# Kernel optimization log

Hardware: AMD Instinct MI355X
Metric: run time of the kernel (lower is better)

The kernel has to match this reference:

```python
import jax, jax.numpy as jnp
import numpy as np

D_MODEL = 1024
N_HEAD = 16
D_K = D_MODEL // N_HEAD


def setup_inputs() -> dict:
    key = jax.random.key(0)
    ks = jax.random.split(key, 11)
    B, S = 2, 2048
    std = 1.0 / np.sqrt(D_MODEL)
    inp = {
        "Q": jax.random.normal(ks[0], (B, S, D_MODEL), jnp.float32),
        "K": jax.random.normal(ks[1], (B, S, D_MODEL), jnp.float32),
        "V": jax.random.normal(ks[2], (B, S, D_MODEL), jnp.float32),
        "Wq": jax.random.normal(ks[3], (D_MODEL, D_MODEL), jnp.float32) * std,
        "bq": jnp.zeros((D_MODEL,), jnp.float32),
        "Wk": jax.random.normal(ks[4], (D_MODEL, D_MODEL), jnp.float32) * std,
        "bk": jnp.zeros((D_MODEL,), jnp.float32),
        "Wv": jax.random.normal(ks[5], (D_MODEL, D_MODEL), jnp.float32) * std,
        "bv": jnp.zeros((D_MODEL,), jnp.float32),
        "Wo": jax.random.normal(ks[6], (D_MODEL, D_MODEL), jnp.float32) * std,
        "bo": jnp.zeros((D_MODEL,), jnp.float32),
    }
    return inp


def _split_heads(x):
    # [B, S, D] -> [B, H, S, d_k]
    B, S, _ = x.shape
    return x.reshape(B, S, N_HEAD, D_K).transpose(0, 2, 1, 3)


def reference(Q, K, V, Wq, bq, Wk, bk, Wv, bv, Wo, bo):
    q = _split_heads(Q @ Wq.T + bq)   # [B,H,S,dk]
    k = _split_heads(K @ Wk.T + bk)
    v = _split_heads(V @ Wv.T + bv)
    scale = 1.0 / jnp.sqrt(jnp.float32(D_K))
    scores = jnp.einsum("bhqd,bhkd->bhqk", q, k) * scale
    attn = jax.nn.softmax(scores, axis=-1)
    ctx = jnp.einsum("bhqk,bhkd->bhqd", attn, v)  # [B,H,S,dk]
    B, H, S, dk = ctx.shape
    ctx = ctx.transpose(0, 2, 1, 3).reshape(B, S, H * dk)
    return ctx @ Wo.T + bo
```

## Files before the change

### kernel.cpp

```cpp
#include <hip/hip_runtime.h>
#include <hip/hip_bf16.h>
#include <cstdint>
#include <cstddef>
#include <cmath>

typedef __attribute__((ext_vector_type(8))) short short8;
typedef __attribute__((ext_vector_type(4))) short short4_t;
typedef __attribute__((ext_vector_type(4))) float f32x4;
typedef __attribute__((ext_vector_type(16))) float f32x16;

constexpr int B_ = 2, S_ = 2048, H_ = 16, DK_ = 64, DM_ = 1024;

__device__ inline unsigned short f2bf(float x) {
  union { float f; unsigned u; } c; c.f = x;
  unsigned r = c.u + 0x7FFF + ((c.u >> 16) & 1);
  return (unsigned short)(r >> 16);
}

__device__ inline float ex2(float x) {
#if __has_builtin(__builtin_amdgcn_exp2f)
  return __builtin_amdgcn_exp2f(x);
#else
  return exp2f(x);
#endif
}

__device__ inline unsigned pkbf(float lo, float hi) {
  unsigned u;
  asm("v_cvt_pk_bf16_f32 %0, %1, %2" : "=v"(u) : "v"(lo), "v"(hi));
  return u;
}

__device__ inline void plswap(unsigned& a, unsigned& b) {
#if __has_builtin(__builtin_amdgcn_permlane32_swap)
  auto r = __builtin_amdgcn_permlane32_swap(a, b, false, false);
  a = (unsigned)r[0];
  b = (unsigned)r[1];
#else
  unsigned sa = __shfl_xor(a, 32), sb = __shfl_xor(b, 32);
  unsigned lid = __builtin_amdgcn_mbcnt_hi(~0u, __builtin_amdgcn_mbcnt_lo(~0u, 0));
  bool hi = lid >= 32;
  unsigned na = hi ? sb : a;
  unsigned nb = hi ? b : sa;
  a = na; b = nb;
#endif
}

__device__ inline float red_half_max(float x) {
  unsigned a = __float_as_uint(x), b = a;
  plswap(a, b);
  return fmaxf(__uint_as_float(a), __uint_as_float(b));
}
__device__ inline float red_half_sum(float x) {
  unsigned a = __float_as_uint(x), b = a;
  plswap(a, b);
  return __uint_as_float(a) + __uint_as_float(b);
}

__device__ inline f32x4 mfma16(short8 a, short8 b, f32x4 c) {
  return __builtin_amdgcn_mfma_f32_16x16x32_bf16(a, b, c, 0, 0, 0);
}
__device__ inline f32x16 mfma32(short8 a, short8 b, f32x16 c) {
  return __builtin_amdgcn_mfma_f32_32x32x16_bf16(a, b, c, 0, 0, 0);
}

__device__ inline void glds16(const unsigned short* g, unsigned short* l) {
  __builtin_amdgcn_global_load_lds(
      (const __attribute__((address_space(1))) unsigned int*)g,
      (__attribute__((address_space(3))) unsigned int*)l, 16, 0, 0);
}

__global__ __launch_bounds__(256) void cvt_all(
    const float* __restrict__ Q, const float* __restrict__ K,
    const float* __restrict__ V, const float* __restrict__ Wq,
    const float* __restrict__ Wk, const float* __restrict__ Wv,
    const float* __restrict__ Wo, unsigned short* __restrict__ Qb,
    unsigned short* __restrict__ Kb, unsigned short* __restrict__ Vb,
    unsigned short* __restrict__ Wqb, unsigned short* __restrict__ Wkb,
    unsigned short* __restrict__ Wvb, unsigned short* __restrict__ Wob) {
  int bid = blockIdx.x;
  const float* in; unsigned short* out; int off;
  if (bid < 4096)       { in = Q;  out = Qb;  off = bid; }
  else if (bid < 8192)  { in = K;  out = Kb;  off = bid - 4096; }
  else if (bid < 12288) { in = V;  out = Vb;  off = bid - 8192; }
  else if (bid < 13312) { in = Wq; out = Wqb; off = bid - 12288; }
  else if (bid < 14336) { in = Wk; out = Wkb; off = bid - 13312; }
  else if (bid < 15360) { in = Wv; out = Wvb; off = bid - 14336; }
  else                  { in = Wo; out = Wob; off = bid - 15360; }
  int i = off * 256 + threadIdx.x;
  float4 f = ((const float4*)in)[i];
  uint2 o;
  o.x = pkbf(f.x, f.y);
  o.y = pkbf(f.z, f.w);
  ((uint2*)out)[i] = o;
}

__device__ inline void store_out(float* p, float v) { *p = v; }
__device__ inline void store_out(unsigned short* p, float v) { *p = f2bf(v); }

template <typename OUT_T>
__device__ inline void gemm128_body(const unsigned short* __restrict__ A,
                                    const unsigned short* __restrict__ Bw,
                                    const float* __restrict__ bias,
                                    OUT_T* __restrict__ C, float cscale,
                                    int bm, int bn) {
  constexpr int Kd = 1024, Nd = 1024;
  __shared__ unsigned short As[128][64];
  __shared__ unsigned short Bs[128][64];

  const int tid = threadIdx.x;
  const int lane = tid & 63, wave = tid >> 6;
  const int li = lane & 15, lg = lane >> 4;
  const int wm = wave >> 1, wn = wave & 1;

  const f32x4 zero4 = {0.f, 0.f, 0.f, 0.f};
  f32x4 acc[4][4];
#pragma unroll
  for (int i = 0; i < 4; i++)
#pragma unroll
    for (int j = 0; j < 4; j++) acc[i][j] = zero4;

  const int srow = tid >> 3;
  const int scol = (tid & 7) * 8;
  const unsigned short* Ag = A + (size_t)(bm * 128 + srow) * Kd + scol;
  const unsigned short* Bg = Bw + (size_t)(bn * 128 + srow) * Kd + scol;

  for (int kt = 0; kt < Kd; kt += 64) {
#pragma unroll
    for (int i = 0; i < 4; i++) {
      glds16(Ag + (size_t)(i * 32) * Kd + kt, &As[i * 32 + srow][scol]);
      glds16(Bg + (size_t)(i * 32) * Kd + kt, &Bs[i * 32 + srow][scol]);
    }
    __syncthreads();

    short8 af[4][2], bf[4][2];
#pragma unroll
    for (int kb = 0; kb < 2; kb++)
#pragma unroll
      for (int i = 0; i < 4; i++) {
        af[i][kb] = *(const short8*)&As[wm * 64 + i * 16 + li][kb * 32 + lg * 8];
        bf[i][kb] = *(const short8*)&Bs[wn * 64 + i * 16 + li][kb * 32 + lg * 8];
      }
#pragma unroll
    for (int kb = 0; kb < 2; kb++)
#pragma unroll
      for (int i = 0; i < 4; i++)
#pragma unroll
        for (int j = 0; j < 4; j++)
          acc[i][j] = mfma16(af[i][kb], bf[j][kb], acc[i][j]);
    __syncthreads();
  }

#pragma unroll
  for (int j = 0; j < 4; j++) {
    int col = bn * 128 + wn * 64 + j * 16 + li;
    float bv = bias[col];
#pragma unroll
    for (int i = 0; i < 4; i++) {
      int row0 = bm * 128 + wm * 64 + i * 16 + lg * 4;
#pragma unroll
      for (int r = 0; r < 4; r++)
        store_out(&C[(size_t)(row0 + r) * Nd + col], (acc[i][j][r] + bv) * cscale);
    }
  }
}

__global__ __launch_bounds__(256) void gemm_qkv(
    const unsigned short* __restrict__ Aq, const unsigned short* __restrict__ Ak,
    const unsigned short* __restrict__ Av, const unsigned short* __restrict__ Bq,
    const unsigned short* __restrict__ Bk, const unsigned short* __restrict__ Bv,
    const float* __restrict__ bq, const float* __restrict__ bk,
    const float* __restrict__ bv, unsigned short* __restrict__ Cq,
    unsigned short* __restrict__ Ck, unsigned short* __restrict__ Cv,
    float qscale) {
  const int z = blockIdx.z;
  const unsigned short* A = z == 0 ? Aq : z == 1 ? Ak : Av;
  const unsigned short* Bw = z == 0 ? Bq : z == 1 ? Bk : Bv;
  const float* bi = z == 0 ? bq : z == 1 ? bk : bv;
  unsigned short* C = z == 0 ? Cq : z == 1 ? Ck : Cv;
  gemm128_body(A, Bw, bi, C, z == 0 ? qscale : 1.0f, blockIdx.x, blockIdx.y);
}

__device__ inline void gemm_body(const unsigned short* __restrict__ A,
                                 const unsigned short* __restrict__ Bw,
                                 const float* __restrict__ bias,
                                 float* __restrict__ C, int bm, int bn) {
  constexpr int Kd = 1024, Nd = 1024, NSTEP = Kd / 64;
  __shared__ unsigned short As[2][128][64];
  __shared__ unsigned short Bs[2][64][64];

  const int tid = threadIdx.x;
  const int lane = tid & 63, wave = tid >> 6;
  const int li = lane & 15, lg = lane >> 4;
  const int wm = wave >> 1, wn = wave & 1;

  const f32x4 zero4 = {0.f, 0.f, 0.f, 0.f};
  f32x4 acc[4][2];
#pragma unroll
  for (int i = 0; i < 4; i++)
#pragma unroll
    for (int j = 0; j < 2; j++) acc[i][j] = zero4;

  const int stg_row = tid >> 3;
  const int stg_col = (tid & 7) * 8;
  const unsigned short* Ag = A + (size_t)(bm * 128 + stg_row) * Kd + stg_col;
  const unsigned short* Bg = Bw + (size_t)(bn * 64 + stg_row) * Kd + stg_col;

#pragma unroll
  for (int i = 0; i < 4; i++)
    glds16(Ag + (size_t)(i * 32) * Kd, &As[0][i * 32 + stg_row][stg_col]);
#pragma unroll
  for (int i = 0; i < 2; i++)
    glds16(Bg + (size_t)(i * 32) * Kd, &Bs[0][i * 32 + stg_row][stg_col]);

  for (int kt = 0; kt < NSTEP; kt++) {
    const int buf = kt & 1;
    asm volatile("s_waitcnt vmcnt(0)" ::: "memory");
    __builtin_amdgcn_sched_barrier(0);
    __builtin_amdgcn_s_barrier();
    __builtin_amdgcn_sched_barrier(0);

    if (kt + 1 < NSTEP) {
      const int kof = (kt + 1) * 64;
#pragma unroll
      for (int i = 0; i < 4; i++)
        glds16(Ag + (size_t)(i * 32) * Kd + kof,
               &As[buf ^ 1][i * 32 + stg_row][stg_col]);
#pragma unroll
      for (int i = 0; i < 2; i++)
        glds16(Bg + (size_t)(i * 32) * Kd + kof,
               &Bs[buf ^ 1][i * 32 + stg_row][stg_col]);
    }
    __builtin_amdgcn_sched_barrier(0);

    short8 af[4][2], bf[2][2];
#pragma unroll
    for (int kb = 0; kb < 2; kb++) {
#pragma unroll
      for (int i = 0; i < 4; i++)
        af[i][kb] =
            *(const short8*)&As[buf][wm * 64 + i * 16 + li][kb * 32 + lg * 8];
#pragma unroll
      for (int j = 0; j < 2; j++)
        bf[j][kb] =
            *(const short8*)&Bs[buf][wn * 32 + j * 16 + li][kb * 32 + lg * 8];
    }
#pragma unroll
    for (int kb = 0; kb < 2; kb++)
#pragma unroll
      for (int i = 0; i < 4; i++)
#pragma unroll
        for (int j = 0; j < 2; j++)
          acc[i][j] = mfma16(af[i][kb], bf[j][kb], acc[i][j]);
  }

#pragma unroll
  for (int j = 0; j < 2; j++) {
    int col = bn * 64 + wn * 32 + j * 16 + li;
    float bv = bias[col];
#pragma unroll
    for (int i = 0; i < 4; i++) {
      int row0 = bm * 128 + wm * 64 + i * 16 + lg * 4;
#pragma unroll
      for (int r = 0; r < 4; r++)
        store_out(&C[(size_t)(row0 + r) * Nd + col], acc[i][j][r] + bv);
    }
  }
}

__global__ __launch_bounds__(256, 3) void gemm_out(
    const unsigned short* __restrict__ A, const unsigned short* __restrict__ Bw,
    const float* __restrict__ bias, float* __restrict__ C) {
  gemm_body(A, Bw, bias, C, blockIdx.x, blockIdx.y);
}

struct V4 { short8 v[4]; };

__device__ __forceinline__ void attn_tile_step(
    int kt, int buf, int NT,
    const unsigned short* kg, const unsigned short* vg,
    unsigned short* KsAll, unsigned short* VtAll,
    int srow, int sc, int scs, int key2, int dq,
    const short8* qf, int l31, int h,
    V4& vc, V4& vn, f32x16* po, float& m_i, float& l_i) {
  unsigned short* KsB = KsAll + buf * (128 * 64);
  unsigned short* VtB = VtAll + buf * (64 * 128);
  unsigned short* KsO = KsAll + (buf ^ 1) * (128 * 64);

  asm volatile("s_waitcnt vmcnt(0)" ::: "memory");
  __builtin_amdgcn_sched_barrier(0);

#pragma unroll
  for (int j = 0; j < 16; j++) {
    const int half = j >> 3, jj = j & 7;
    unsigned w = (unsigned)(unsigned short)vc.v[half][jj] |
                 ((unsigned)(unsigned short)vc.v[2 + half][jj] << 16);
    const int slot = (key2 >> 3) ^ j;
    *(unsigned*)&VtB[(dq * 16 + j) * 128 + slot * 8 + (key2 & 7)] = w;
  }

  if (kt + 1 < NT) {
    const unsigned short* vp =
        vg + (size_t)((kt + 1) * 128 + key2) * DM_ + dq * 16;
    vn.v[0] = *(const short8*)(vp);
    vn.v[1] = *(const short8*)(vp + 8);
    vn.v[2] = *(const short8*)(vp + DM_);
    vn.v[3] = *(const short8*)(vp + DM_ + 8);
  }

  asm volatile("s_waitcnt lgkmcnt(0)" ::: "memory");
  __builtin_amdgcn_sched_barrier(0);
  __builtin_amdgcn_s_barrier();
  __builtin_amdgcn_sched_barrier(0);

  if (kt + 1 < NT) {
    const unsigned short* kgt = kg + (size_t)((kt + 1) * 128) * DM_;
#pragma unroll
    for (int i = 0; i < 4; i++)
      glds16(kgt + (size_t)(i * 32 + srow) * DM_ + scs,
             &KsO[(i * 32 + srow) * 64 + sc * 8]);
  }
  __builtin_amdgcn_sched_barrier(0);

  f32x16 sacc[4];
#pragma unroll
  for (int kb = 0; kb < 4; kb++)
#pragma unroll
    for (int r = 0; r < 16; r++) sacc[kb][r] = 0.f;

  __builtin_amdgcn_s_setprio(1);
#pragma unroll
  for (int tq = 0; tq < 4; tq++) {
    const int sl = ((((tq << 1) | h) ^ (l31 & 7))) * 8;
#pragma unroll
    for (int kb = 0; kb < 4; kb++) {
      short8 kf = *(const short8*)&KsB[(kb * 32 + l31) * 64 + sl];
      sacc[kb] = mfma32(kf, qf[tq], sacc[kb]);
    }
  }
  __builtin_amdgcn_s_setprio(0);

  float mx = -1e30f;
#pragma unroll
  for (int kb = 0; kb < 4; kb++)
#pragma unroll
    for (int r = 0; r < 16; r += 4)
      mx = fmaxf(mx, fmaxf(fmaxf(sacc[kb][r], sacc[kb][r + 1]),
                           fmaxf(sacc[kb][r + 2], sacc[kb][r + 3])));
  mx = red_half_max(mx);

  if (!__all(mx - m_i <= 8.0f)) {
    float mn = fmaxf(m_i, mx);
    float al = ex2(m_i - mn);
    m_i = mn;
    l_i *= al;
#pragma unroll
    for (int db = 0; db < 2; db++)
#pragma unroll
      for (int r = 0; r < 16; r++) po[db][r] *= al;
  }

  float s0 = 0.f, s1 = 0.f, s2 = 0.f, s3 = 0.f;
#pragma unroll
  for (int kb = 0; kb < 4; kb++) {
#pragma unroll
    for (int r = 0; r < 16; r += 4) {
      float p0 = ex2(sacc[kb][r] - m_i);
      float p1 = ex2(sacc[kb][r + 1] - m_i);
      float p2 = ex2(sacc[kb][r + 2] - m_i);
      float p3 = ex2(sacc[kb][r + 3] - m_i);
      sacc[kb][r] = p0; sacc[kb][r + 1] = p1;
      sacc[kb][r + 2] = p2; sacc[kb][r + 3] = p3;
      s0 += p0; s1 += p1; s2 += p2; s3 += p3;
    }
    unsigned u[4][2];
#pragma unroll
    for (int qd = 0; qd < 4; qd++) {
      u[qd][0] = pkbf(sacc[kb][4 * qd], sacc[kb][4 * qd + 1]);
      u[qd][1] = pkbf(sacc[kb][4 * qd + 2], sacc[kb][4 * qd + 3]);
    }
    __builtin_amdgcn_s_setprio(1);
#pragma unroll
    for (int tt = 0; tt < 2; tt++) {
      const int tp = 2 * kb + tt;
      unsigned x0 = u[2 * tt][0], x1 = u[2 * tt][1];
      unsigned y0 = u[2 * tt + 1][0], y1 = u[2 * tt + 1][1];
      plswap(x0, y0);
      plswap(x1, y1);
      union { unsigned w[4]; short8 v8; } fr;
      fr.w[0] = x0;
      fr.w[1] = x1;
      fr.w[2] = y0;
      fr.w[3] = y1;
      const int slbase = (tp << 1) | h;
#pragma unroll
      for (int db = 0; db < 2; db++) {
        const int row = db * 32 + l31;
        short8 vf = *(const short8*)
            &VtB[row * 128 + (slbase ^ (l31 & 15)) * 8];
        po[db] = mfma32(vf, fr.v8, po[db]);
      }
    }
    __builtin_amdgcn_s_setprio(0);
  }
  float sum = (s0 + s1) + (s2 + s3);
  l_i += red_half_sum(sum);
}

__global__ __launch_bounds__(256, 2) void attn_fwd(
    const unsigned short* __restrict__ q, const unsigned short* __restrict__ k,
    const unsigned short* __restrict__ v, unsigned short* __restrict__ ctx) {
  __shared__ unsigned short Ks[2][128][64];
  __shared__ unsigned short Vt[2][64][128];

  const int tid = threadIdx.x;
  const int lane = tid & 63, wave = tid >> 6;
  const int l31 = lane & 31, h = lane >> 5;
  const int n = blockIdx.x;
  const int xcd = n & 7, m = n >> 3;
  const int bh = xcd * 4 + (m & 3);
  const int qt = m >> 2;
  const int b = bh >> 4, hd = bh & 15;

  const int qrow = qt * 128 + wave * 32 + l31;
  const unsigned short* qg = q + (size_t)(b * S_ + qrow) * DM_ + hd * DK_;
  short8 qf[4];
#pragma unroll
  for (int t = 0; t < 4; t++) qf[t] = *(const short8*)(qg + t * 16 + h * 8);

  f32x16 po[2];
#pragma unroll
  for (int db = 0; db < 2; db++)
#pragma unroll
    for (int r = 0; r < 16; r++) po[db][r] = 0.f;
  float m_i = -1e30f, l_i = 0.f;

  const int srow = tid >> 3, sc = tid & 7;
  const int scs = (sc ^ (srow & 7)) * 8;
  const unsigned short* kg = k + (size_t)(b * S_) * DM_ + hd * DK_;

  const int key2 = (tid & 63) * 2, dq = tid >> 6;
  const unsigned short* vg = v + (size_t)(b * S_) * DM_ + hd * DK_;

  const int NT = S_ / 128;

#pragma unroll
  for (int i = 0; i < 4; i++)
    glds16(kg + (size_t)(i * 32 + srow) * DM_ + scs,
           &Ks[0][i * 32 + srow][sc * 8]);
  V4 va, vb;
  {
    const unsigned short* vp = vg + (size_t)key2 * DM_ + dq * 16;
    va.v[0] = *(const short8*)(vp);
    va.v[1] = *(const short8*)(vp + 8);
    va.v[2] = *(const short8*)(vp + DM_);
    va.v[3] = *(const short8*)(vp + DM_ + 8);
  }

  unsigned short* KsAll = &Ks[0][0][0];
  unsigned short* VtAll = &Vt[0][0][0];
  for (int it = 0; it < NT; it += 2) {
    attn_tile_step(it, 0, NT, kg, vg, KsAll, VtAll, srow, sc, scs, key2, dq,
                   qf, l31, h, va, vb, po, m_i, l_i);
    attn_tile_step(it + 1, 1, NT, kg, vg, KsAll, VtAll, srow, sc, scs, key2,
                   dq, qf, l31, h, vb, va, po, m_i, l_i);
  }

  float rl = 1.0f / l_i;
  unsigned short* cg = ctx + (size_t)(b * S_ + qrow) * DM_ + hd * DK_;
#pragma unroll
  for (int db = 0; db < 2; db++)
#pragma unroll
    for (int rq = 0; rq < 4; rq++) {
      uint2 w2;
      w2.x = pkbf(po[db][4 * rq] * rl, po[db][4 * rq + 1] * rl);
      w2.y = pkbf(po[db][4 * rq + 2] * rl, po[db][4 * rq + 3] * rl);
      *(uint2*)(cg + db * 32 + 8 * rq + 4 * h) = w2;
    }
}

extern "C" void kernel_launch(void* const* d_in, const int* in_sizes, int n_in,
                              void* d_out, int out_size, void* d_ws, size_t ws_size,
                              hipStream_t stream) {
  const float* Q  = (const float*)d_in[0];
  const float* Kx = (const float*)d_in[1];
  const float* V  = (const float*)d_in[2];
  const float* Wq = (const float*)d_in[3];
  const float* bq = (const float*)d_in[4];
  const float* Wk = (const float*)d_in[5];
  const float* bk = (const float*)d_in[6];
  const float* Wv = (const float*)d_in[7];
  const float* bv = (const float*)d_in[8];
  const float* Wo = (const float*)d_in[9];
  const float* bo = (const float*)d_in[10];
  float* out = (float*)d_out;

  char* ws = (char*)d_ws;
  const size_t MB = 1ull << 20;
  unsigned short* Qb  = (unsigned short*)(ws + 0 * MB);
  unsigned short* Kb  = (unsigned short*)(ws + 8 * MB);
  unsigned short* Vb  = (unsigned short*)(ws + 16 * MB);
  unsigned short* Wqb = (unsigned short*)(ws + 24 * MB);
  unsigned short* Wkb = (unsigned short*)(ws + 26 * MB);
  unsigned short* Wvb = (unsigned short*)(ws + 28 * MB);
  unsigned short* Wob = (unsigned short*)(ws + 30 * MB);
  unsigned short* qp  = (unsigned short*)(ws + 32 * MB);
  unsigned short* kp  = (unsigned short*)(ws + 40 * MB);
  unsigned short* vp  = (unsigned short*)(ws + 48 * MB);
  unsigned short* cx  = (unsigned short*)(ws + 56 * MB);

  cvt_all<<<16384, 256, 0, stream>>>(Q, Kx, V, Wq, Wk, Wv, Wo,
                                     Qb, Kb, Vb, Wqb, Wkb, Wvb, Wob);

  gemm_qkv<<<dim3(32, 8, 3), 256, 0, stream>>>(
      Qb, Kb, Vb, Wqb, Wkb, Wvb, bq, bk, bv, qp, kp, vp, 0.18033688f);

  attn_fwd<<<512, 256, 0, stream>>>(qp, kp, vp, cx);

  gemm_out<<<dim3(32, 16), 256, 0, stream>>>(cx, Wob, bo, out);
}
```

Before: 135.8 us.

## Split attention key tiles across two wave groups per block with LDS merge

The attention kernel now launches 512 threads per block. Two groups of four waves each process half of every 128-key tile for the same 128 query rows, which halves per-wave MFMA and softmax work per tile. Each group keeps its own running max and sum. The partial outputs are merged through LDS at the end using a log-sum-exp rescale. This adds a final sync and merge step plus extra registers per block, and it aims to raise the number of waves per CU to hide latency.

```diff
diff --git a/kernel.cpp b/kernel.cpp
--- a/kernel.cpp
+++ b/kernel.cpp
@@ -274,15 +274,15 @@
   gemm_body(A, Bw, bias, C, blockIdx.x, blockIdx.y);
 }
 
-struct V4 { short8 v[4]; };
+struct V2 { short8 v[2]; };
 
 __device__ __forceinline__ void attn_tile_step(
     int kt, int buf, int NT,
     const unsigned short* kg, const unsigned short* vg,
     unsigned short* KsAll, unsigned short* VtAll,
     int srow, int sc, int scs, int key2, int dq,
-    const short8* qf, int l31, int h,
-    V4& vc, V4& vn, f32x16* po, float& m_i, float& l_i) {
+    const short8* qf, int l31, int h, int grp,
+    V2& vc, V2& vn, f32x16* po, float& m_i, float& l_i) {
   unsigned short* KsB = KsAll + buf * (128 * 64);
   unsigned short* VtB = VtAll + buf * (64 * 128);
   unsigned short* KsO = KsAll + (buf ^ 1) * (128 * 64);
@@ -291,21 +291,19 @@
   __builtin_amdgcn_sched_barrier(0);
 
 #pragma unroll
-  for (int j = 0; j < 16; j++) {
-    const int half = j >> 3, jj = j & 7;
-    unsigned w = (unsigned)(unsigned short)vc.v[half][jj] |
-                 ((unsigned)(unsigned short)vc.v[2 + half][jj] << 16);
-    const int slot = (key2 >> 3) ^ j;
-    *(unsigned*)&VtB[(dq * 16 + j) * 128 + slot * 8 + (key2 & 7)] = w;
+  for (int j = 0; j < 8; j++) {
+    unsigned w = (unsigned)(unsigned short)vc.v[0][j] |
+                 ((unsigned)(unsigned short)vc.v[1][j] << 16);
+    const int row = dq * 8 + j;
+    const int slot = (key2 >> 3) ^ (row & 15);
+    *(unsigned*)&VtB[row * 128 + slot * 8 + (key2 & 7)] = w;
   }
 
   if (kt + 1 < NT) {
     const unsigned short* vp =
-        vg + (size_t)((kt + 1) * 128 + key2) * DM_ + dq * 16;
+        vg + (size_t)((kt + 1) * 128 + key2) * DM_ + dq * 8;
     vn.v[0] = *(const short8*)(vp);
-    vn.v[1] = *(const short8*)(vp + 8);
-    vn.v[2] = *(const short8*)(vp + DM_);
-    vn.v[3] = *(const short8*)(vp + DM_ + 8);
+    vn.v[1] = *(const short8*)(vp + DM_);
   }
 
   asm volatile("s_waitcnt lgkmcnt(0)" ::: "memory");
@@ -315,16 +313,15 @@
 
   if (kt + 1 < NT) {
     const unsigned short* kgt = kg + (size_t)((kt + 1) * 128) * DM_;
-#pragma unroll
-    for (int i = 0; i < 4; i++)
-      glds16(kgt + (size_t)(i * 32 + srow) * DM_ + scs,
-             &KsO[(i * 32 + srow) * 64 + sc * 8]);
+    glds16(kgt + (size_t)srow * DM_ + scs, &KsO[srow * 64 + sc * 8]);
+    glds16(kgt + (size_t)(64 + srow) * DM_ + scs,
+           &KsO[(64 + srow) * 64 + sc * 8]);
   }
   __builtin_amdgcn_sched_barrier(0);
 
-  f32x16 sacc[4];
-#pragma unroll
-  for (int kb = 0; kb < 4; kb++)
+  f32x16 sacc[2];
+#pragma unroll
+  for (int kb = 0; kb < 2; kb++)
 #pragma unroll
     for (int r = 0; r < 16; r++) sacc[kb][r] = 0.f;
 
@@ -333,8 +330,8 @@
   for (int tq = 0; tq < 4; tq++) {
     const int sl = ((((tq << 1) | h) ^ (l31 & 7))) * 8;
 #pragma unroll
-    for (int kb = 0; kb < 4; kb++) {
-      short8 kf = *(const short8*)&KsB[(kb * 32 + l31) * 64 + sl];
+    for (int kb = 0; kb < 2; kb++) {
+      short8 kf = *(const short8*)&KsB[(grp * 64 + kb * 32 + l31) * 64 + sl];
       sacc[kb] = mfma32(kf, qf[tq], sacc[kb]);
     }
   }
@@ -342,7 +339,7 @@
 
   float mx = -1e30f;
 #pragma unroll
-  for (int kb = 0; kb < 4; kb++)
+  for (int kb = 0; kb < 2; kb++)
 #pragma unroll
     for (int r = 0; r < 16; r += 4)
       mx = fmaxf(mx, fmaxf(fmaxf(sacc[kb][r], sacc[kb][r + 1]),
@@ -362,7 +359,7 @@
 
   float s0 = 0.f, s1 = 0.f, s2 = 0.f, s3 = 0.f;
 #pragma unroll
-  for (int kb = 0; kb < 4; kb++) {
+  for (int kb = 0; kb < 2; kb++) {
 #pragma unroll
     for (int r = 0; r < 16; r += 4) {
       float p0 = ex2(sacc[kb][r] - m_i);
@@ -382,7 +379,7 @@
     __builtin_amdgcn_s_setprio(1);
 #pragma unroll
     for (int tt = 0; tt < 2; tt++) {
-      const int tp = 2 * kb + tt;
+      const int tp = grp * 4 + 2 * kb + tt;
       unsigned x0 = u[2 * tt][0], x1 = u[2 * tt][1];
       unsigned y0 = u[2 * tt + 1][0], y1 = u[2 * tt + 1][1];
       plswap(x0, y0);
@@ -407,7 +404,7 @@
   l_i += red_half_sum(sum);
 }
 
-__global__ __launch_bounds__(256, 2) void attn_fwd(
+__global__ __launch_bounds__(512, 4) void attn_fwd(
     const unsigned short* __restrict__ q, const unsigned short* __restrict__ k,
     const unsigned short* __restrict__ v, unsigned short* __restrict__ ctx) {
   __shared__ unsigned short Ks[2][128][64];
@@ -416,13 +413,14 @@
   const int tid = threadIdx.x;
   const int lane = tid & 63, wave = tid >> 6;
   const int l31 = lane & 31, h = lane >> 5;
+  const int grp = wave >> 2, qsub = wave & 3;
   const int n = blockIdx.x;
   const int xcd = n & 7, m = n >> 3;
   const int bh = xcd * 4 + (m & 3);
   const int qt = m >> 2;
   const int b = bh >> 4, hd = bh & 15;
 
-  const int qrow = qt * 128 + wave * 32 + l31;
+  const int qrow = qt * 128 + qsub * 32 + l31;
   const unsigned short* qg = q + (size_t)(b * S_ + qrow) * DM_ + hd * DK_;
   short8 qf[4];
 #pragma unroll
@@ -444,39 +442,64 @@
 
   const int NT = S_ / 128;
 
-#pragma unroll
-  for (int i = 0; i < 4; i++)
-    glds16(kg + (size_t)(i * 32 + srow) * DM_ + scs,
-           &Ks[0][i * 32 + srow][sc * 8]);
-  V4 va, vb;
+  glds16(kg + (size_t)srow * DM_ + scs, &Ks[0][srow][sc * 8]);
+  glds16(kg + (size_t)(64 + srow) * DM_ + scs, &Ks[0][64 + srow][sc * 8]);
+  V2 va, vb;
   {
-    const unsigned short* vp = vg + (size_t)key2 * DM_ + dq * 16;
+    const unsigned short* vp = vg + (size_t)key2 * DM_ + dq * 8;
     va.v[0] = *(const short8*)(vp);
-    va.v[1] = *(const short8*)(vp + 8);
-    va.v[2] = *(const short8*)(vp + DM_);
-    va.v[3] = *(const short8*)(vp + DM_ + 8);
+    va.v[1] = *(const short8*)(vp + DM_);
   }
 
   unsigned short* KsAll = &Ks[0][0][0];
   unsigned short* VtAll = &Vt[0][0][0];
   for (int it = 0; it < NT; it += 2) {
     attn_tile_step(it, 0, NT, kg, vg, KsAll, VtAll, srow, sc, scs, key2, dq,
-                   qf, l31, h, va, vb, po, m_i, l_i);
+                   qf, l31, h, grp, va, vb, po, m_i, l_i);
     attn_tile_step(it + 1, 1, NT, kg, vg, KsAll, VtAll, srow, sc, scs, key2,
-                   dq, qf, l31, h, vb, va, po, m_i, l_i);
-  }
-
-  float rl = 1.0f / l_i;
-  unsigned short* cg = ctx + (size_t)(b * S_ + qrow) * DM_ + hd * DK_;
-#pragma unroll
-  for (int db = 0; db < 2; db++)
-#pragma unroll
-    for (int rq = 0; rq < 4; rq++) {
-      uint2 w2;
-      w2.x = pkbf(po[db][4 * rq] * rl, po[db][4 * rq + 1] * rl);
-      w2.y = pkbf(po[db][4 * rq + 2] * rl, po[db][4 * rq + 3] * rl);
-      *(uint2*)(cg + db * 32 + 8 * rq + 4 * h) = w2;
-    }
+                   dq, qf, l31, h, grp, vb, va, po, m_i, l_i);
+  }
+
+  __syncthreads();
+  float* poL = (float*)VtAll;
+  float* mL = (float*)KsAll;
+  float* lL = mL + 256;
+  const int gid = qsub * 64 + lane;
+  if (grp == 1) {
+#pragma unroll
+    for (int db = 0; db < 2; db++)
+#pragma unroll
+      for (int r = 0; r < 16; r++) {
+        int j = db * 16 + r;
+        poL[gid * 32 + (j ^ (gid & 31))] = po[db][r];
+      }
+    mL[gid] = m_i;
+    lL[gid] = l_i;
+  }
+  __syncthreads();
+  if (grp == 0) {
+    float mB = mL[gid], lB = lL[gid];
+    float mm = fmaxf(m_i, mB);
+    float aA = ex2(m_i - mm), aB = ex2(mB - mm);
+    float rl = 1.0f / (l_i * aA + lB * aB);
+    unsigned short* cg = ctx + (size_t)(b * S_ + qrow) * DM_ + hd * DK_;
+#pragma unroll
+    for (int db = 0; db < 2; db++)
+#pragma unroll
+      for (int rq = 0; rq < 4; rq++) {
+        float vv[4];
+#pragma unroll
+        for (int kk = 0; kk < 4; kk++) {
+          int j = db * 16 + 4 * rq + kk;
+          vv[kk] = (po[db][4 * rq + kk] * aA +
+                    poL[gid * 32 + (j ^ (gid & 31))] * aB) * rl;
+        }
+        uint2 w2;
+        w2.x = pkbf(vv[0], vv[1]);
+        w2.y = pkbf(vv[2], vv[3]);
+        *(uint2*)(cg + db * 32 + 8 * rq + 4 * h) = w2;
+      }
+  }
 }
 
 extern "C" void kernel_launch(void* const* d_in, const int* in_sizes, int n_in,
@@ -515,7 +538,7 @@
   gemm_qkv<<<dim3(32, 8, 3), 256, 0, stream>>>(
       Qb, Kb, Vb, Wqb, Wkb, Wvb, bq, bk, bv, qp, kp, vp, 0.18033688f);
 
-  attn_fwd<<<512, 256, 0, stream>>>(qp, kp, vp, cx);
+  attn_fwd<<<512, 512, 0, stream>>>(qp, kp, vp, cx);
 
   gemm_out<<<dim3(32, 16), 256, 0, stream>>>(cx, Wob, bo, out);
 }
```

Measured after the change: 140.9 us. +3.8%, slower.

## Defer the P·V MFMA of each attention tile into the next tile step

Applied to the files above, without the earlier changes.

The attention loop is software-pipelined. Each tile's softmax probabilities are packed to bf16 and held in registers, and the P·V matrix multiply is applied at the start of the next tile step, reading from the other V buffer. A final P·V pass runs after the loop. The goal is to overlap P·V MFMA work with the global loads, the LDS transpose and the QK^T/softmax of the following tile, so the exp/softmax VALU work no longer sits between dependent MFMA chains. In exchange it holds about 32 extra VGPRs for the packed probabilities and relies on the existing barrier ordering to keep the double-buffered V tile valid one step longer.

```diff
diff --git a/kernel.cpp b/kernel.cpp
--- a/kernel.cpp
+++ b/kernel.cpp
@@ -275,6 +275,38 @@
 }
 
 struct V4 { short8 v[4]; };
+struct PPack { unsigned u[4][4][2]; };
+
+__device__ __forceinline__ void pv_apply(const PPack& pk,
+                                         const unsigned short* VtO,
+                                         int l31, int h, f32x16* po) {
+  __builtin_amdgcn_s_setprio(1);
+#pragma unroll
+  for (int kb = 0; kb < 4; kb++) {
+#pragma unroll
+    for (int tt = 0; tt < 2; tt++) {
+      const int tp = 2 * kb + tt;
+      unsigned x0 = pk.u[kb][2 * tt][0], x1 = pk.u[kb][2 * tt][1];
+      unsigned y0 = pk.u[kb][2 * tt + 1][0], y1 = pk.u[kb][2 * tt + 1][1];
+      plswap(x0, y0);
+      plswap(x1, y1);
+      union { unsigned w[4]; short8 v8; } fr;
+      fr.w[0] = x0;
+      fr.w[1] = x1;
+      fr.w[2] = y0;
+      fr.w[3] = y1;
+      const int slbase = (tp << 1) | h;
+#pragma unroll
+      for (int db = 0; db < 2; db++) {
+        const int row = db * 32 + l31;
+        short8 vf = *(const short8*)
+            &VtO[row * 128 + (slbase ^ (l31 & 15)) * 8];
+        po[db] = mfma32(vf, fr.v8, po[db]);
+      }
+    }
+  }
+  __builtin_amdgcn_s_setprio(0);
+}
 
 __device__ __forceinline__ void attn_tile_step(
     int kt, int buf, int NT,
@@ -282,10 +314,12 @@
     unsigned short* KsAll, unsigned short* VtAll,
     int srow, int sc, int scs, int key2, int dq,
     const short8* qf, int l31, int h,
-    V4& vc, V4& vn, f32x16* po, float& m_i, float& l_i) {
+    V4& vc, V4& vn, PPack& pprev, PPack& pcur,
+    f32x16* po, float& m_i, float& l_i) {
   unsigned short* KsB = KsAll + buf * (128 * 64);
   unsigned short* VtB = VtAll + buf * (64 * 128);
   unsigned short* KsO = KsAll + (buf ^ 1) * (128 * 64);
+  unsigned short* VtO = VtAll + (buf ^ 1) * (64 * 128);
 
   asm volatile("s_waitcnt vmcnt(0)" ::: "memory");
   __builtin_amdgcn_sched_barrier(0);
@@ -307,6 +341,8 @@
     vn.v[2] = *(const short8*)(vp + DM_);
     vn.v[3] = *(const short8*)(vp + DM_ + 8);
   }
+
+  if (kt > 0) pv_apply(pprev, VtO, l31, h, po);
 
   asm volatile("s_waitcnt lgkmcnt(0)" ::: "memory");
   __builtin_amdgcn_sched_barrier(0);
@@ -373,35 +409,11 @@
       sacc[kb][r + 2] = p2; sacc[kb][r + 3] = p3;
       s0 += p0; s1 += p1; s2 += p2; s3 += p3;
     }
-    unsigned u[4][2];
 #pragma unroll
     for (int qd = 0; qd < 4; qd++) {
-      u[qd][0] = pkbf(sacc[kb][4 * qd], sacc[kb][4 * qd + 1]);
-      u[qd][1] = pkbf(sacc[kb][4 * qd + 2], sacc[kb][4 * qd + 3]);
-    }
-    __builtin_amdgcn_s_setprio(1);
-#pragma unroll
-    for (int tt = 0; tt < 2; tt++) {
-      const int tp = 2 * kb + tt;
-      unsigned x0 = u[2 * tt][0], x1 = u[2 * tt][1];
-      unsigned y0 = u[2 * tt + 1][0], y1 = u[2 * tt + 1][1];
-      plswap(x0, y0);
-      plswap(x1, y1);
-      union { unsigned w[4]; short8 v8; } fr;
-      fr.w[0] = x0;
-      fr.w[1] = x1;
-      fr.w[2] = y0;
-      fr.w[3] = y1;
-      const int slbase = (tp << 1) | h;
-#pragma unroll
-      for (int db = 0; db < 2; db++) {
-        const int row = db * 32 + l31;
-        short8 vf = *(const short8*)
-            &VtB[row * 128 + (slbase ^ (l31 & 15)) * 8];
-        po[db] = mfma32(vf, fr.v8, po[db]);
-      }
-    }
-    __builtin_amdgcn_s_setprio(0);
+      pcur.u[kb][qd][0] = pkbf(sacc[kb][4 * qd], sacc[kb][4 * qd + 1]);
+      pcur.u[kb][qd][1] = pkbf(sacc[kb][4 * qd + 2], sacc[kb][4 * qd + 3]);
+    }
   }
   float sum = (s0 + s1) + (s2 + s3);
   l_i += red_half_sum(sum);
@@ -459,12 +471,14 @@
 
   unsigned short* KsAll = &Ks[0][0][0];
   unsigned short* VtAll = &Vt[0][0][0];
+  PPack pA, pB;
   for (int it = 0; it < NT; it += 2) {
     attn_tile_step(it, 0, NT, kg, vg, KsAll, VtAll, srow, sc, scs, key2, dq,
-                   qf, l31, h, va, vb, po, m_i, l_i);
+                   qf, l31, h, va, vb, pB, pA, po, m_i, l_i);
     attn_tile_step(it + 1, 1, NT, kg, vg, KsAll, VtAll, srow, sc, scs, key2,
-                   dq, qf, l31, h, vb, va, po, m_i, l_i);
-  }
+                   dq, qf, l31, h, vb, va, pA, pB, po, m_i, l_i);
+  }
+  pv_apply(pB, VtAll + 1 * (64 * 128), l31, h, po);
 
   float rl = 1.0f / l_i;
   unsigned short* cg = ctx + (size_t)(b * S_ + qrow) * DM_ + hd * DK_;
```

Measured after the change: 137.2 us. No clear change (+1.0%).
